# Optimization experiments

Measured on AMD Instinct MI355X. Metric: run time of the kernel, lower is better.

## Reference

```python
import math
import jax, jax.numpy as jnp
import numpy as np

ALPHA, BETA, GAMMA = 1.9, 3.8, 15.2
HEIGHT, WIDTH, SKIP = 32, 32, 1
NUM_HEADS, DIM = 12, 768
HEAD_DIM = DIM // NUM_HEADS


def _piecewise_index_np(rp, alpha, beta, gamma):
    # Eq. (18): identity inside |rp|<=alpha, logarithmic bucketing outside, clipped at beta.
    rp = rp.astype(np.float64)
    rp_abs = np.abs(rp)
    inside = np.round(rp)
    log_part = alpha + np.log(np.maximum(rp_abs, 1e-9) / alpha) / math.log(gamma / alpha) * (beta - alpha)
    outside = np.sign(rp) * np.minimum(np.round(log_part), beta)
    return np.where(rp_abs <= alpha, inside, outside).astype(np.int64)


def _bucket_ids_cross(height, width, skip, alpha, beta, gamma, axis):
    # axis=0 -> CROSS_ROWS, axis=1 -> CROSS_COLS
    rows = np.arange(height)[:, None].repeat(width, 1)
    cols = np.arange(width)[None, :].repeat(height, 0)
    pos = np.stack([rows, cols], 2).reshape(-1, 2)  # [L, 2]
    diff = pos[:, None, axis] - pos[None, :, axis]  # [L, L]
    beta_int = int(beta)
    ids = _piecewise_index_np(diff, alpha, beta, gamma) + beta_int  # in [0, 2*beta_int]
    num_buckets = 2 * beta_int + 1
    L = height * width
    if skip > 0:
        extra = num_buckets
        new_ids = np.full((skip + L, skip + L), extra, dtype=np.int64)
        new_ids[skip:, skip:] = ids
        ids = new_ids
        num_buckets += 1
    return ids.astype(np.int32), num_buckets


def setup_inputs() -> dict:
    key = jax.random.key(0)
    ks = jax.random.split(key, 8)
    N = SKIP + HEIGHT * WIDTH  # 1025
    B = 8
    br, nb = _bucket_ids_cross(HEIGHT, WIDTH, SKIP, ALPHA, BETA, GAMMA, axis=0)
    bc, _ = _bucket_ids_cross(HEIGHT, WIDTH, SKIP, ALPHA, BETA, GAMMA, axis=1)
    w = 0.02
    return {
        "x": jax.random.normal(ks[0], (B, N, DIM), jnp.float32),
        "qkv_w": jax.random.normal(ks[1], (3 * DIM, DIM), jnp.float32) * w,
        "qkv_b": jnp.zeros((3 * DIM,), jnp.float32),
        "proj_w": jax.random.normal(ks[2], (DIM, DIM), jnp.float32) * w,
        "proj_b": jnp.zeros((DIM,), jnp.float32),
        "rpe_rows": jax.random.normal(ks[3], (NUM_HEADS, nb, HEAD_DIM), jnp.float32) * w,
        "rpe_cols": jax.random.normal(ks[4], (NUM_HEADS, nb, HEAD_DIM), jnp.float32) * w,
        "bucket_rows": jnp.asarray(br),
        "bucket_cols": jnp.asarray(bc),
    }


def reference(x, qkv_w, qkv_b, proj_w, proj_b, rpe_rows, rpe_cols, bucket_rows, bucket_cols):
    B, N, C = x.shape
    h = rpe_rows.shape[0]
    d = C // h
    scale = d ** -0.5
    qkv = (x @ qkv_w.T + qkv_b).reshape(B, N, 3, h, d).transpose(2, 0, 3, 1, 4)  # [3,B,h,N,d]
    q, k, v = qkv[0] * scale, qkv[1], qkv[2]
    attn = jnp.einsum('bhid,bhjd->bhij', q, k)  # [B,h,N,N]
    # contextual RPE on keys: project q onto per-head bucket tables, gather per (i,j)
    qt_r = jnp.einsum('bhid,hud->bhiu', q, rpe_rows)  # [B,h,N,nb]
    qt_c = jnp.einsum('bhid,hud->bhiu', q, rpe_cols)
    bias = (jnp.take_along_axis(qt_r, bucket_rows[None, None].astype(jnp.int32), axis=3)
            + jnp.take_along_axis(qt_c, bucket_cols[None, None].astype(jnp.int32), axis=3))
    attn = jax.nn.softmax(attn + bias, axis=-1)
    out = jnp.einsum('bhij,bhjd->bhid', attn, v)
    out = out.transpose(0, 2, 1, 3).reshape(B, N, C)
    return out @ proj_w.T + proj_b
```

## Files before the change

kernel.cpp:

```cpp
#include <hip/hip_runtime.h>

typedef unsigned short u16;
typedef unsigned int   u32;
typedef short  s16x8 __attribute__((ext_vector_type(8)));
typedef float  f32x4 __attribute__((ext_vector_type(4)));

#define B_   8
#define N_   1025
#define H_   12
#define D_   64
#define C_   768
#define NB_  8
#define M_   (B_*N_)
#define QKV_ (3*C_)
#define NEGI -30000.0f
#define LOG2E 1.44269504089f
#define SHIFT2 11.5415603271f
#define CS_  1088

__device__ __forceinline__ float bf2f(u16 u) {
    unsigned int i = ((unsigned int)u) << 16;
    float f; __builtin_memcpy(&f, &i, 4); return f;
}
__device__ __forceinline__ u16 f2bf(float f) {
    unsigned int i; __builtin_memcpy(&i, &f, 4);
    i = (i + 0x7FFFu + ((i >> 16) & 1u)) >> 16;
    return (u16)i;
}
__device__ __forceinline__ float exp2fast(float x) {
#if __has_builtin(__builtin_amdgcn_exp2f)
    return __builtin_amdgcn_exp2f(x);
#else
    float r; asm("v_exp_f32 %0, %1" : "=v"(r) : "v"(x)); return r;
#endif
}

__device__ __forceinline__ void gload_lds16(const u16* gptr, u16* lptr) {
    __builtin_amdgcn_global_load_lds(
        (const __attribute__((address_space(1))) void*)gptr,
        (__attribute__((address_space(3))) void*)lptr, 16, 0, 0);
}

__global__ __launch_bounds__(256)
void cvt_f32_bf16(const float* __restrict__ a, u16* __restrict__ oa, long na,
                  const float* __restrict__ b, u16* __restrict__ ob, long nb,
                  const float* __restrict__ c, u16* __restrict__ oc, long nc)
{
    long t = ((long)blockIdx.x * 256 + threadIdx.x) * 8;
    const float* s; u16* d; long off;
    if (t < na)                 { s = a; d = oa; off = t; }
    else if (t < na + nb)       { s = b; d = ob; off = t - na; }
    else if (t < na + nb + nc)  { s = c; d = oc; off = t - na - nb; }
    else return;
    float4 f0 = *reinterpret_cast<const float4*>(s + off);
    float4 f1 = *reinterpret_cast<const float4*>(s + off + 4);
    u16 tmp[8] = { f2bf(f0.x), f2bf(f0.y), f2bf(f0.z), f2bf(f0.w),
                   f2bf(f1.x), f2bf(f1.y), f2bf(f1.z), f2bf(f1.w) };
    *reinterpret_cast<uint4*>(d + off) = *reinterpret_cast<uint4*>(tmp);
}

__global__ void build_cidx(const int* __restrict__ brow, const int* __restrict__ bcol,
                           unsigned char* __restrict__ cidx) {
    long t = (long)blockIdx.x * 256 + threadIdx.x;
    const long total = (long)CS_ * (CS_ / 4);
    if (t >= total) return;
    int i = (int)(t / (CS_ / 4));
    int k = (int)(t % (CS_ / 4));
    u32 w = 0;
    int p0 = k * 4;
    #pragma unroll
    for (int bnb = 0; bnb < 4; ++bnb) {
        int p = p0 + bnb;
        int jt = p >> 6, rem = p & 63;
        int l = rem >> 2, bn = rem & 3;
        int j = jt * 64 + bn * 16 + l;
        u32 c = 63u;
        if (i < N_ && j < N_) {
            u32 br = (u32)(brow[(size_t)i * N_ + j] & 7);
            u32 bc = (u32)(bcol[(size_t)i * N_ + j] & 7);
            c = (br << 3) | bc;
        }
        w |= c << (8 * bnb);
    }
    ((u32*)cidx)[t] = w;
}

template<int OF32>
__global__ __launch_bounds__(256)
void gemm_bt(const u16* __restrict__ Ap, int lda,
             const u16* __restrict__ Btp,
             const float* __restrict__ bias,
             void* __restrict__ Cout, int ldc,
             int M, int Nn, int K, int scale_cols, float scale_val)
{
    __shared__ u16 As[128][32];
    __shared__ u16 Bs[128][32];
    const int tid  = threadIdx.x;
    const int lane = tid & 63;
    const int wave = tid >> 6;
    const int wm = (wave >> 1) * 64;
    const int wn = (wave & 1) * 64;
    const int m0 = blockIdx.y * 128;
    const int n0 = blockIdx.x * 128;

    const int srow = wave * 16 + (lane >> 2);
    const int scol = (lane & 3) * 8;

    f32x4 acc[4][4] = {};

    for (int k0 = 0; k0 < K; k0 += 32) {
        __syncthreads();
        #pragma unroll
        for (int i = 0; i < 2; ++i) {
            int ar = m0 + i * 64 + srow;
            if (ar > M - 1) ar = M - 1;
            gload_lds16(Ap + (size_t)ar * lda + k0 + scol, &As[i * 64 + wave * 16][0]);
            int br = n0 + i * 64 + srow;
            gload_lds16(Btp + (size_t)br * K + k0 + scol,  &Bs[i * 64 + wave * 16][0]);
        }
        __syncthreads();

        s16x8 af[4], bfv[4];
        #pragma unroll
        for (int qq = 0; qq < 4; ++qq) {
            af[qq]  = *reinterpret_cast<const s16x8*>(&As[wm + qq*16 + (lane & 15)][(lane >> 4) * 8]);
            bfv[qq] = *reinterpret_cast<const s16x8*>(&Bs[wn + qq*16 + (lane & 15)][(lane >> 4) * 8]);
        }
        #pragma unroll
        for (int bm = 0; bm < 4; ++bm)
            #pragma unroll
            for (int bn = 0; bn < 4; ++bn)
                acc[bm][bn] = __builtin_amdgcn_mfma_f32_16x16x32_bf16(af[bm], bfv[bn], acc[bm][bn], 0, 0, 0);
    }

    #pragma unroll
    for (int bm = 0; bm < 4; ++bm) {
        #pragma unroll
        for (int bn = 0; bn < 4; ++bn) {
            int col = n0 + wn + bn*16 + (lane & 15);
            float bv = bias[col];
            float sc = (col < scale_cols) ? scale_val : 1.0f;
            #pragma unroll
            for (int r = 0; r < 4; ++r) {
                int row = m0 + wm + bm*16 + (lane >> 4)*4 + r;
                if (row < M) {
                    float v = (acc[bm][bn][r] + bv) * sc;
                    size_t idx = (size_t)row * ldc + col;
                    if (OF32) ((float*)Cout)[idx] = v;
                    else      ((u16*)Cout)[idx]   = f2bf(v);
                }
            }
        }
    }
}

__global__ __launch_bounds__(256)
void flash_kernel(const u16* __restrict__ qkv,
                  const float* __restrict__ rpe_r, const float* __restrict__ rpe_c,
                  const unsigned char* __restrict__ cidx,
                  u16* __restrict__ aout)
{
    __shared__ u16 Ks[64][72];
    __shared__ u16 Vt[64][72];
    __shared__ u16 Ps[4][16][72];
    __shared__ u16 qtComb[64][72];

    const int tid  = threadIdx.x;
    const int lane = tid & 63;
    const int wave = tid >> 6;
    const int q    = lane >> 4;
    const int l    = lane & 15;
    const int bh = blockIdx.y;
    const int b = bh / H_;
    const int h = bh % H_;
    const int i0 = blockIdx.x * 64;

    float* qtrA = (float*)&Ps[0][0][0];
    float* qtcA = qtrA + 64 * 8;

    {
        int row = tid >> 2;
        int u0  = (tid & 3) * 2;
        int ig = i0 + row;
        float qv[64];
        if (ig < N_) {
            const u16* qrow = &qkv[(size_t)(b * N_ + ig) * QKV_ + h * D_];
            #pragma unroll
            for (int e = 0; e < 8; ++e) {
                uint4 t = *reinterpret_cast<const uint4*>(&qrow[e * 8]);
                s16x8 q8 = *reinterpret_cast<s16x8*>(&t);
                #pragma unroll
                for (int j = 0; j < 8; ++j) qv[e*8 + j] = bf2f((u16)q8[j]);
            }
        } else {
            #pragma unroll
            for (int d = 0; d < 64; ++d) qv[d] = 0.f;
        }
        #pragma unroll
        for (int uu = 0; uu < 2; ++uu) {
            int u = u0 + uu;
            const float4* rr4 = (const float4*)&rpe_r[(size_t)(h * NB_ + u) * D_];
            const float4* rc4 = (const float4*)&rpe_c[(size_t)(h * NB_ + u) * D_];
            float sr = 0.f, sc = 0.f;
            #pragma unroll
            for (int e = 0; e < 16; ++e) {
                float4 a = rr4[e], c4 = rc4[e];
                sr += qv[4*e]*a.x + qv[4*e+1]*a.y + qv[4*e+2]*a.z + qv[4*e+3]*a.w;
                sc += qv[4*e]*c4.x + qv[4*e+1]*c4.y + qv[4*e+2]*c4.z + qv[4*e+3]*c4.w;
            }
            qtrA[row*8 + u] = sr;
            qtcA[row*8 + u] = sc;
        }
    }
    __syncthreads();
    {
        int row = tid >> 2;
        int c0  = (tid & 3) * 16;
        u16 tmp[16];
        #pragma unroll
        for (int cc = 0; cc < 16; ++cc) {
            int c = c0 + cc;
            tmp[cc] = f2bf(qtrA[row*8 + (c >> 3)] + qtcA[row*8 + (c & 7)]);
        }
        *reinterpret_cast<uint4*>(&qtComb[row][c0])     = *reinterpret_cast<uint4*>(&tmp[0]);
        *reinterpret_cast<uint4*>(&qtComb[row][c0 + 8]) = *reinterpret_cast<uint4*>(&tmp[8]);
    }

    s16x8 qf[2];
    {
        int iq = i0 + wave * 16 + l;
        #pragma unroll
        for (int ks = 0; ks < 2; ++ks) {
            uint4 v = make_uint4(0u, 0u, 0u, 0u);
            if (iq < N_)
                v = *reinterpret_cast<const uint4*>(
                    &qkv[(size_t)(b * N_ + iq) * QKV_ + h * D_ + ks * 32 + q * 8]);
            qf[ks] = *reinterpret_cast<s16x8*>(&v);
        }
    }

    float l_part[4] = {0.f, 0.f, 0.f, 0.f};
    f32x4 o_acc[4] = {};

    const int srow = tid >> 3;
    const int g8   = tid & 7;
    const int scol = g8 * 8;
    const int rowq  = wave * 16 + q * 4;
    const int rowq4 = q * 4;

    uint4 kpre[2], vpre[2];
    #pragma unroll
    for (int rr = 0; rr < 2; ++rr) {
        int jg = rr * 32 + srow;
        kpre[rr] = make_uint4(0u,0u,0u,0u); vpre[rr] = make_uint4(0u,0u,0u,0u);
        if (jg < N_) {
            size_t base = (size_t)(b * N_ + jg) * QKV_ + h * D_ + scol;
            kpre[rr] = *reinterpret_cast<const uint4*>(&qkv[base + C_]);
            vpre[rr] = *reinterpret_cast<const uint4*>(&qkv[base + 2 * C_]);
        }
    }

#define SMAX_BN(bn, MASKED_)                                                  \
    {                                                                         \
        const int jbw = (((bn) << 1) | (l >> 3)) ^ q;                         \
        const int sw = (jbw << 3) | (l & 7);                                  \
        _Pragma("unroll")                                                     \
        for (int r = 0; r < 4; ++r) {                                         \
            int c = (cpk[r] >> ((bn) * 8)) & 63;                              \
            float biasv = bf2f(qtComb[rowq + r][c]);                          \
            float lg = s[bn][r] + biasv;                                      \
            if (MASKED_) { if ((j0 + (bn) * 16 + l) >= N_) lg = NEGI; }       \
            float p = exp2fast(lg);                                           \
            l_part[r] += p;                                                   \
            Ps[wave][rowq4 + r][sw] = f2bf(p);                                \
        }                                                                     \
    }

#define PVHALF(ks)                                                            \
    {                                                                         \
        const int qi = (l >> 2) & 3;                                          \
        s16x8 pf = *reinterpret_cast<const s16x8*>(                           \
            &Ps[wave][l][((((ks) << 2) | q) ^ qi) << 3]);                     \
        _Pragma("unroll")                                                     \
        for (int bn = 0; bn < 4; ++bn) {                                      \
            int gd = ((bn << 1) | (l >> 3)) & 7;                              \
            int jb = (((ks) << 2) | q) ^ gd;                                  \
            s16x8 vf = *reinterpret_cast<const s16x8*>(&Vt[bn * 16 + l][jb << 3]); \
            o_acc[bn] = __builtin_amdgcn_mfma_f32_16x16x32_bf16(pf, vf, o_acc[bn], 0, 0, 0); \
        }                                                                     \
    }

    const int nJT = (N_ + 63) / 64;
    for (int jt = 0; jt < nJT; ++jt) {
        const int j0 = jt * 64;

        u32 cpk[4];
        #pragma unroll
        for (int r = 0; r < 4; ++r) {
            int ig = i0 + wave * 16 + q * 4 + r;
            cpk[r] = *reinterpret_cast<const u32*>(&cidx[(size_t)ig * CS_ + j0 + 4 * l]);
        }

        __syncthreads();

        #pragma unroll
        for (int rr = 0; rr < 2; ++rr) {
            int row = rr * 32 + srow;
            *reinterpret_cast<uint4*>(&Ks[row][scol]) = kpre[rr];
            s16x8 v8 = *reinterpret_cast<s16x8*>(&vpre[rr]);
            int base = (((row >> 3) ^ g8) << 3) | (row & 7);
            #pragma unroll
            for (int e = 0; e < 8; ++e) Vt[scol + e][base] = (u16)v8[e];
        }
        #pragma unroll
        for (int rr = 0; rr < 2; ++rr) {
            int jg = (jt + 1) * 64 + rr * 32 + srow;
            kpre[rr] = make_uint4(0u,0u,0u,0u); vpre[rr] = make_uint4(0u,0u,0u,0u);
            if (jg < N_) {
                size_t base = (size_t)(b * N_ + jg) * QKV_ + h * D_ + scol;
                kpre[rr] = *reinterpret_cast<const uint4*>(&qkv[base + C_]);
                vpre[rr] = *reinterpret_cast<const uint4*>(&qkv[base + 2 * C_]);
            }
        }
        __syncthreads();

        f32x4 s[4];
        #pragma unroll
        for (int bn = 0; bn < 4; ++bn)
            s[bn] = (f32x4){-SHIFT2, -SHIFT2, -SHIFT2, -SHIFT2};
        #pragma unroll
        for (int bn = 0; bn < 4; ++bn) {
            #pragma unroll
            for (int ks = 0; ks < 2; ++ks) {
                s16x8 kf = *reinterpret_cast<const s16x8*>(&Ks[bn * 16 + l][ks * 32 + q * 8]);
                s[bn] = __builtin_amdgcn_mfma_f32_16x16x32_bf16(qf[ks], kf, s[bn], 0, 0, 0);
            }
        }

        if (jt < nJT - 1) {
            SMAX_BN(0, 0) SMAX_BN(1, 0)
            PVHALF(0)
            SMAX_BN(2, 0) SMAX_BN(3, 0)
            PVHALF(1)
        } else {
            SMAX_BN(0, 1) SMAX_BN(1, 1)
            PVHALF(0)
            SMAX_BN(2, 1) SMAX_BN(3, 1)
            PVHALF(1)
        }
    }

    #pragma unroll
    for (int r = 0; r < 4; ++r) {
        #pragma unroll
        for (int s2 = 1; s2 < 16; s2 <<= 1)
            l_part[r] += __shfl_xor(l_part[r], s2, 64);
    }
    #pragma unroll
    for (int bn = 0; bn < 4; ++bn) {
        #pragma unroll
        for (int r = 0; r < 4; ++r) {
            int ig = i0 + wave * 16 + q * 4 + r;
            if (ig < N_) {
                float lsum = l_part[r];
                float invl = (lsum > 0.f) ? (1.0f / lsum) : 0.f;
                aout[(size_t)(b * N_ + ig) * C_ + h * D_ + bn * 16 + l] = f2bf(o_acc[bn][r] * invl);
            }
        }
    }
#undef SMAX_BN
#undef PVHALF
}

extern "C" void kernel_launch(void* const* d_in, const int* in_sizes, int n_in,
                              void* d_out, int out_size, void* d_ws, size_t ws_size,
                              hipStream_t stream)
{
    const float* x      = (const float*)d_in[0];
    const float* qkv_w  = (const float*)d_in[1];
    const float* qkv_b  = (const float*)d_in[2];
    const float* proj_w = (const float*)d_in[3];
    const float* proj_b = (const float*)d_in[4];
    const float* rpe_r  = (const float*)d_in[5];
    const float* rpe_c  = (const float*)d_in[6];
    const int*   brow   = (const int*)d_in[7];
    const int*   bcol   = (const int*)d_in[8];

    char* p = (char*)d_ws;
    u16* qkv  = (u16*)p; p += (size_t)M_ * QKV_ * 2;
    u16* xaout = (u16*)p; p += (size_t)M_ * C_ * 2;
    unsigned char* cidx = (unsigned char*)p; p += (size_t)CS_ * CS_;
    u16* w1bf = (u16*)p; p += (size_t)QKV_ * C_ * 2;
    u16* w2bf = (u16*)p;

    const long nx = (long)M_ * C_;
    const long n1 = (long)QKV_ * C_;
    const long n2 = (long)C_ * C_;

    cvt_f32_bf16<<<(int)((nx + n1 + n2) / 8 / 256), 256, 0, stream>>>(
        x, xaout, nx, qkv_w, w1bf, n1, proj_w, w2bf, n2);

    build_cidx<<<((CS_ * (CS_ / 4)) + 255) / 256, 256, 0, stream>>>(brow, bcol, cidx);

    gemm_bt<0><<<dim3(QKV_ / 128, (M_ + 127) / 128), 256, 0, stream>>>(
        xaout, C_, w1bf, qkv_b, qkv, QKV_, M_, QKV_, C_, C_, 0.125f * LOG2E);

    flash_kernel<<<dim3((N_ + 63) / 64, B_ * H_), 256, 0, stream>>>(
        qkv, rpe_r, rpe_c, cidx, xaout);

    gemm_bt<1><<<dim3(C_ / 128, (M_ + 127) / 128), 256, 0, stream>>>(
        xaout, C_, w2bf, proj_b, d_out, C_, M_, C_, C_, 0, 1.0f);
}
```

Measured before the change: 328.8 us.

## Write V transposed from QKV GEMM and read K/V fragments directly from global

The QKV GEMM epilogue now writes V into a separate transposed, padded [B,H,D,1088] buffer and keeps Q and K in a narrower 1536-wide array. The flash kernel drops its shared-memory K and V staging, the register prefetch and two barriers per tile, and loads MFMA fragments straight from global memory (L2/L1). This is meant to remove the LDS transpose and sync cost. In exchange the GEMM does strided scattered stores for V, a small extra kernel zeroes the padding, and global load latency is no longer hidden by prefetching.

Result: slower. 513.5 us (+56.2%).

```diff
diff --git a/kernel.cpp b/kernel.cpp
--- a/kernel.cpp
+++ b/kernel.cpp
@@ -13,6 +13,8 @@
 #define NB_  8
 #define M_   (B_*N_)
 #define QKV_ (3*C_)
+#define QK2_ 1536
+#define VS2_ 1088
 #define NEGI -30000.0f
 #define LOG2E 1.44269504089f
 #define SHIFT2 11.5415603271f
@@ -57,6 +59,16 @@
     u16 tmp[8] = { f2bf(f0.x), f2bf(f0.y), f2bf(f0.z), f2bf(f0.w),
                    f2bf(f1.x), f2bf(f1.y), f2bf(f1.z), f2bf(f1.w) };
     *reinterpret_cast<uint4*>(d + off) = *reinterpret_cast<uint4*>(tmp);
+}
+
+__global__ __launch_bounds__(256)
+void zero_vpad(u16* __restrict__ vT) {
+    const int pad = VS2_ - N_;
+    int t = blockIdx.x * 256 + threadIdx.x;
+    const int total = B_ * H_ * D_ * pad;
+    if (t >= total) return;
+    int rr = t / pad, pp = t % pad;
+    vT[(size_t)rr * VS2_ + N_ + pp] = 0;
 }
 
 __global__ void build_cidx(const int* __restrict__ brow, const int* __restrict__ bcol,
@@ -85,13 +97,14 @@
     ((u32*)cidx)[t] = w;
 }
 
-template<int OF32>
+template<int OF32, int VT>
 __global__ __launch_bounds__(256)
 void gemm_bt(const u16* __restrict__ Ap, int lda,
              const u16* __restrict__ Btp,
              const float* __restrict__ bias,
              void* __restrict__ Cout, int ldc,
-             int M, int Nn, int K, int scale_cols, float scale_val)
+             int M, int Nn, int K, int scale_cols, float scale_val,
+             u16* __restrict__ vt)
 {
     __shared__ u16 As[128][32];
     __shared__ u16 Bs[128][32];
@@ -145,9 +158,16 @@
                 int row = m0 + wm + bm*16 + (lane >> 4)*4 + r;
                 if (row < M) {
                     float v = (acc[bm][bn][r] + bv) * sc;
-                    size_t idx = (size_t)row * ldc + col;
-                    if (OF32) ((float*)Cout)[idx] = v;
-                    else      ((u16*)Cout)[idx]   = f2bf(v);
+                    if (VT && col >= 2 * C_) {
+                        int b2 = row / N_;
+                        int j2 = row - b2 * N_;
+                        int hd = col - 2 * C_;
+                        vt[((size_t)(b2 * (H_ * D_) + hd)) * VS2_ + j2] = f2bf(v);
+                    } else {
+                        size_t idx = (size_t)row * ldc + col;
+                        if (OF32) ((float*)Cout)[idx] = v;
+                        else      ((u16*)Cout)[idx]   = f2bf(v);
+                    }
                 }
             }
         }
@@ -156,12 +176,11 @@
 
 __global__ __launch_bounds__(256)
 void flash_kernel(const u16* __restrict__ qkv,
+                  const u16* __restrict__ vT,
                   const float* __restrict__ rpe_r, const float* __restrict__ rpe_c,
                   const unsigned char* __restrict__ cidx,
                   u16* __restrict__ aout)
 {
-    __shared__ u16 Ks[64][72];
-    __shared__ u16 Vt[64][72];
     __shared__ u16 Ps[4][16][72];
     __shared__ u16 qtComb[64][72];
 
@@ -182,20 +201,8 @@
         int row = tid >> 2;
         int u0  = (tid & 3) * 2;
         int ig = i0 + row;
-        float qv[64];
-        if (ig < N_) {
-            const u16* qrow = &qkv[(size_t)(b * N_ + ig) * QKV_ + h * D_];
-            #pragma unroll
-            for (int e = 0; e < 8; ++e) {
-                uint4 t = *reinterpret_cast<const uint4*>(&qrow[e * 8]);
-                s16x8 q8 = *reinterpret_cast<s16x8*>(&t);
-                #pragma unroll
-                for (int j = 0; j < 8; ++j) qv[e*8 + j] = bf2f((u16)q8[j]);
-            }
-        } else {
-            #pragma unroll
-            for (int d = 0; d < 64; ++d) qv[d] = 0.f;
-        }
+        bool valid = ig < N_;
+        const u16* qrow = &qkv[(size_t)(b * N_ + (valid ? ig : 0)) * QK2_ + h * D_];
         #pragma unroll
         for (int uu = 0; uu < 2; ++uu) {
             int u = u0 + uu;
@@ -203,13 +210,22 @@
             const float4* rc4 = (const float4*)&rpe_c[(size_t)(h * NB_ + u) * D_];
             float sr = 0.f, sc = 0.f;
             #pragma unroll
-            for (int e = 0; e < 16; ++e) {
-                float4 a = rr4[e], c4 = rc4[e];
-                sr += qv[4*e]*a.x + qv[4*e+1]*a.y + qv[4*e+2]*a.z + qv[4*e+3]*a.w;
-                sc += qv[4*e]*c4.x + qv[4*e+1]*c4.y + qv[4*e+2]*c4.z + qv[4*e+3]*c4.w;
+            for (int e2 = 0; e2 < 8; ++e2) {
+                uint4 t = *reinterpret_cast<const uint4*>(&qrow[e2 * 8]);
+                s16x8 q8 = *reinterpret_cast<s16x8*>(&t);
+                float4 a0 = rr4[2*e2], a1 = rr4[2*e2+1];
+                float4 c0 = rc4[2*e2], c1 = rc4[2*e2+1];
+                float f0 = bf2f((u16)q8[0]), f1 = bf2f((u16)q8[1]);
+                float f2 = bf2f((u16)q8[2]), f3 = bf2f((u16)q8[3]);
+                float f4 = bf2f((u16)q8[4]), f5 = bf2f((u16)q8[5]);
+                float f6 = bf2f((u16)q8[6]), f7 = bf2f((u16)q8[7]);
+                sr += f0*a0.x + f1*a0.y + f2*a0.z + f3*a0.w
+                    + f4*a1.x + f5*a1.y + f6*a1.z + f7*a1.w;
+                sc += f0*c0.x + f1*c0.y + f2*c0.z + f3*c0.w
+                    + f4*c1.x + f5*c1.y + f6*c1.z + f7*c1.w;
             }
-            qtrA[row*8 + u] = sr;
-            qtcA[row*8 + u] = sc;
+            qtrA[row*8 + u] = valid ? sr : 0.f;
+            qtcA[row*8 + u] = valid ? sc : 0.f;
         }
     }
     __syncthreads();
@@ -234,31 +250,20 @@
             uint4 v = make_uint4(0u, 0u, 0u, 0u);
             if (iq < N_)
                 v = *reinterpret_cast<const uint4*>(
-                    &qkv[(size_t)(b * N_ + iq) * QKV_ + h * D_ + ks * 32 + q * 8]);
+                    &qkv[(size_t)(b * N_ + iq) * QK2_ + h * D_ + ks * 32 + q * 8]);
             qf[ks] = *reinterpret_cast<s16x8*>(&v);
         }
     }
+    __syncthreads();
 
     float l_part[4] = {0.f, 0.f, 0.f, 0.f};
     f32x4 o_acc[4] = {};
 
-    const int srow = tid >> 3;
-    const int g8   = tid & 7;
-    const int scol = g8 * 8;
     const int rowq  = wave * 16 + q * 4;
     const int rowq4 = q * 4;
 
-    uint4 kpre[2], vpre[2];
-    #pragma unroll
-    for (int rr = 0; rr < 2; ++rr) {
-        int jg = rr * 32 + srow;
-        kpre[rr] = make_uint4(0u,0u,0u,0u); vpre[rr] = make_uint4(0u,0u,0u,0u);
-        if (jg < N_) {
-            size_t base = (size_t)(b * N_ + jg) * QKV_ + h * D_ + scol;
-            kpre[rr] = *reinterpret_cast<const uint4*>(&qkv[base + C_]);
-            vpre[rr] = *reinterpret_cast<const uint4*>(&qkv[base + 2 * C_]);
-        }
-    }
+    const u16* kb = qkv + (size_t)b * N_ * QK2_ + C_ + h * D_ + q * 8;
+    const u16* vb = vT + ((size_t)(b * H_ + h) * D_) * VS2_ + q * 8;
 
 #define SMAX_BN(bn, MASKED_)                                                  \
     {                                                                         \
@@ -283,9 +288,8 @@
             &Ps[wave][l][((((ks) << 2) | q) ^ qi) << 3]);                     \
         _Pragma("unroll")                                                     \
         for (int bn = 0; bn < 4; ++bn) {                                      \
-            int gd = ((bn << 1) | (l >> 3)) & 7;                              \
-            int jb = (((ks) << 2) | q) ^ gd;                                  \
-            s16x8 vf = *reinterpret_cast<const s16x8*>(&Vt[bn * 16 + l][jb << 3]); \
+            s16x8 vf = *reinterpret_cast<const s16x8*>(                       \
+                vb + (size_t)(bn * 16 + l) * VS2_ + j0 + (ks) * 32);          \
             o_acc[bn] = __builtin_amdgcn_mfma_f32_16x16x32_bf16(pf, vf, o_acc[bn], 0, 0, 0); \
         }                                                                     \
     }
@@ -301,38 +305,18 @@
             cpk[r] = *reinterpret_cast<const u32*>(&cidx[(size_t)ig * CS_ + j0 + 4 * l]);
         }
 
-        __syncthreads();
-
-        #pragma unroll
-        for (int rr = 0; rr < 2; ++rr) {
-            int row = rr * 32 + srow;
-            *reinterpret_cast<uint4*>(&Ks[row][scol]) = kpre[rr];
-            s16x8 v8 = *reinterpret_cast<s16x8*>(&vpre[rr]);
-            int base = (((row >> 3) ^ g8) << 3) | (row & 7);
-            #pragma unroll
-            for (int e = 0; e < 8; ++e) Vt[scol + e][base] = (u16)v8[e];
-        }
-        #pragma unroll
-        for (int rr = 0; rr < 2; ++rr) {
-            int jg = (jt + 1) * 64 + rr * 32 + srow;
-            kpre[rr] = make_uint4(0u,0u,0u,0u); vpre[rr] = make_uint4(0u,0u,0u,0u);
-            if (jg < N_) {
-                size_t base = (size_t)(b * N_ + jg) * QKV_ + h * D_ + scol;
-                kpre[rr] = *reinterpret_cast<const uint4*>(&qkv[base + C_]);
-                vpre[rr] = *reinterpret_cast<const uint4*>(&qkv[base + 2 * C_]);
-            }
-        }
-        __syncthreads();
-
         f32x4 s[4];
         #pragma unroll
         for (int bn = 0; bn < 4; ++bn)
             s[bn] = (f32x4){-SHIFT2, -SHIFT2, -SHIFT2, -SHIFT2};
         #pragma unroll
         for (int bn = 0; bn < 4; ++bn) {
+            int jc = j0 + bn * 16 + l;
+            if (jc >= N_) jc = N_ - 1;
+            const u16* kr = kb + (size_t)jc * QK2_;
             #pragma unroll
             for (int ks = 0; ks < 2; ++ks) {
-                s16x8 kf = *reinterpret_cast<const s16x8*>(&Ks[bn * 16 + l][ks * 32 + q * 8]);
+                s16x8 kf = *reinterpret_cast<const s16x8*>(kr + ks * 32);
                 s[bn] = __builtin_amdgcn_mfma_f32_16x16x32_bf16(qf[ks], kf, s[bn], 0, 0, 0);
             }
         }
@@ -387,8 +371,9 @@
     const int*   bcol   = (const int*)d_in[8];
 
     char* p = (char*)d_ws;
-    u16* qkv  = (u16*)p; p += (size_t)M_ * QKV_ * 2;
+    u16* qkv2  = (u16*)p; p += (size_t)M_ * QK2_ * 2;
     u16* xaout = (u16*)p; p += (size_t)M_ * C_ * 2;
+    u16* vT    = (u16*)p; p += (size_t)B_ * H_ * D_ * VS2_ * 2;
     unsigned char* cidx = (unsigned char*)p; p += (size_t)CS_ * CS_;
     u16* w1bf = (u16*)p; p += (size_t)QKV_ * C_ * 2;
     u16* w2bf = (u16*)p;
@@ -400,14 +385,15 @@
     cvt_f32_bf16<<<(int)((nx + n1 + n2) / 8 / 256), 256, 0, stream>>>(
         x, xaout, nx, qkv_w, w1bf, n1, proj_w, w2bf, n2);
 
+    zero_vpad<<<(B_ * H_ * D_ * (VS2_ - N_) + 255) / 256, 256, 0, stream>>>(vT);
     build_cidx<<<((CS_ * (CS_ / 4)) + 255) / 256, 256, 0, stream>>>(brow, bcol, cidx);
 
-    gemm_bt<0><<<dim3(QKV_ / 128, (M_ + 127) / 128), 256, 0, stream>>>(
-        xaout, C_, w1bf, qkv_b, qkv, QKV_, M_, QKV_, C_, C_, 0.125f * LOG2E);
+    gemm_bt<0,1><<<dim3(QKV_ / 128, (M_ + 127) / 128), 256, 0, stream>>>(
+        xaout, C_, w1bf, qkv_b, qkv2, QK2_, M_, QKV_, C_, C_, 0.125f * LOG2E, vT);
 
     flash_kernel<<<dim3((N_ + 63) / 64, B_ * H_), 256, 0, stream>>>(
-        qkv, rpe_r, rpe_c, cidx, xaout);
-
-    gemm_bt<1><<<dim3(C_ / 128, (M_ + 127) / 128), 256, 0, stream>>>(
-        xaout, C_, w2bf, proj_b, d_out, C_, M_, C_, C_, 0, 1.0f);
-}
+        qkv2, vT, rpe_r, rpe_c, cidx, xaout);
+
+    gemm_bt<1,0><<<dim3(C_ / 128, (M_ + 127) / 128), 256, 0, stream>>>(
+        xaout, C_, w2bf, proj_b, d_out, C_, M_, C_, C_, 0, 1.0f, nullptr);
+}
```

## Double flash attention query tile to 128 rows with 512-thread blocks

Applied to the files above, without the earlier changes.

The flash kernel now processes 128 query rows per block with 8 waves, so each K/V tile staged in shared memory is reused by twice as many query rows and each thread loads one K/V row instead of two. The RPE projection prologue streams q in chunks rather than holding a 64-float register array, which lowers register pressure for the new launch bound of 512 threads with 4 blocks per unit. The cidx row index is clamped to stay in bounds for the larger tile. In exchange the grid has half as many blocks (9 per batch-head) with more padded rows in the last tile, and shared memory per block grows.

After: 316.0 us. 3.9% less time.

```diff
diff --git a/kernel.cpp b/kernel.cpp
--- a/kernel.cpp
+++ b/kernel.cpp
@@ -154,7 +154,7 @@
     }
 }
 
-__global__ __launch_bounds__(256)
+__global__ __launch_bounds__(512, 4)
 void flash_kernel(const u16* __restrict__ qkv,
                   const float* __restrict__ rpe_r, const float* __restrict__ rpe_c,
                   const unsigned char* __restrict__ cidx,
@@ -162,8 +162,8 @@
 {
     __shared__ u16 Ks[64][72];
     __shared__ u16 Vt[64][72];
-    __shared__ u16 Ps[4][16][72];
-    __shared__ u16 qtComb[64][72];
+    __shared__ u16 Ps[8][16][72];
+    __shared__ u16 qtComb[128][72];
 
     const int tid  = threadIdx.x;
     const int lane = tid & 63;
@@ -173,29 +173,17 @@
     const int bh = blockIdx.y;
     const int b = bh / H_;
     const int h = bh % H_;
-    const int i0 = blockIdx.x * 64;
+    const int i0 = blockIdx.x * 128;
 
     float* qtrA = (float*)&Ps[0][0][0];
-    float* qtcA = qtrA + 64 * 8;
+    float* qtcA = qtrA + 128 * 8;
 
     {
         int row = tid >> 2;
         int u0  = (tid & 3) * 2;
         int ig = i0 + row;
-        float qv[64];
-        if (ig < N_) {
-            const u16* qrow = &qkv[(size_t)(b * N_ + ig) * QKV_ + h * D_];
-            #pragma unroll
-            for (int e = 0; e < 8; ++e) {
-                uint4 t = *reinterpret_cast<const uint4*>(&qrow[e * 8]);
-                s16x8 q8 = *reinterpret_cast<s16x8*>(&t);
-                #pragma unroll
-                for (int j = 0; j < 8; ++j) qv[e*8 + j] = bf2f((u16)q8[j]);
-            }
-        } else {
-            #pragma unroll
-            for (int d = 0; d < 64; ++d) qv[d] = 0.f;
-        }
+        bool valid = ig < N_;
+        const u16* qrow = &qkv[(size_t)(b * N_ + (valid ? ig : 0)) * QKV_ + h * D_];
         #pragma unroll
         for (int uu = 0; uu < 2; ++uu) {
             int u = u0 + uu;
@@ -203,13 +191,22 @@
             const float4* rc4 = (const float4*)&rpe_c[(size_t)(h * NB_ + u) * D_];
             float sr = 0.f, sc = 0.f;
             #pragma unroll
-            for (int e = 0; e < 16; ++e) {
-                float4 a = rr4[e], c4 = rc4[e];
-                sr += qv[4*e]*a.x + qv[4*e+1]*a.y + qv[4*e+2]*a.z + qv[4*e+3]*a.w;
-                sc += qv[4*e]*c4.x + qv[4*e+1]*c4.y + qv[4*e+2]*c4.z + qv[4*e+3]*c4.w;
+            for (int e2 = 0; e2 < 8; ++e2) {
+                uint4 t = *reinterpret_cast<const uint4*>(&qrow[e2 * 8]);
+                s16x8 q8 = *reinterpret_cast<s16x8*>(&t);
+                float4 a0 = rr4[2*e2], a1 = rr4[2*e2+1];
+                float4 c0 = rc4[2*e2], c1 = rc4[2*e2+1];
+                float f0 = bf2f((u16)q8[0]), f1 = bf2f((u16)q8[1]);
+                float f2 = bf2f((u16)q8[2]), f3 = bf2f((u16)q8[3]);
+                float f4 = bf2f((u16)q8[4]), f5 = bf2f((u16)q8[5]);
+                float f6 = bf2f((u16)q8[6]), f7 = bf2f((u16)q8[7]);
+                sr += f0*a0.x + f1*a0.y + f2*a0.z + f3*a0.w
+                    + f4*a1.x + f5*a1.y + f6*a1.z + f7*a1.w;
+                sc += f0*c0.x + f1*c0.y + f2*c0.z + f3*c0.w
+                    + f4*c1.x + f5*c1.y + f6*c1.z + f7*c1.w;
             }
-            qtrA[row*8 + u] = sr;
-            qtcA[row*8 + u] = sc;
+            qtrA[row*8 + u] = valid ? sr : 0.f;
+            qtcA[row*8 + u] = valid ? sc : 0.f;
         }
     }
     __syncthreads();
@@ -248,15 +245,14 @@
     const int rowq  = wave * 16 + q * 4;
     const int rowq4 = q * 4;
 
-    uint4 kpre[2], vpre[2];
-    #pragma unroll
-    for (int rr = 0; rr < 2; ++rr) {
-        int jg = rr * 32 + srow;
-        kpre[rr] = make_uint4(0u,0u,0u,0u); vpre[rr] = make_uint4(0u,0u,0u,0u);
+    uint4 kpre, vpre;
+    {
+        int jg = srow;
+        kpre = make_uint4(0u,0u,0u,0u); vpre = make_uint4(0u,0u,0u,0u);
         if (jg < N_) {
             size_t base = (size_t)(b * N_ + jg) * QKV_ + h * D_ + scol;
-            kpre[rr] = *reinterpret_cast<const uint4*>(&qkv[base + C_]);
-            vpre[rr] = *reinterpret_cast<const uint4*>(&qkv[base + 2 * C_]);
+            kpre = *reinterpret_cast<const uint4*>(&qkv[base + C_]);
+            vpre = *reinterpret_cast<const uint4*>(&qkv[base + 2 * C_]);
         }
     }
 
@@ -298,28 +294,26 @@
         #pragma unroll
         for (int r = 0; r < 4; ++r) {
             int ig = i0 + wave * 16 + q * 4 + r;
+            if (ig > CS_ - 1) ig = CS_ - 1;
             cpk[r] = *reinterpret_cast<const u32*>(&cidx[(size_t)ig * CS_ + j0 + 4 * l]);
         }
 
         __syncthreads();
 
-        #pragma unroll
-        for (int rr = 0; rr < 2; ++rr) {
-            int row = rr * 32 + srow;
-            *reinterpret_cast<uint4*>(&Ks[row][scol]) = kpre[rr];
-            s16x8 v8 = *reinterpret_cast<s16x8*>(&vpre[rr]);
-            int base = (((row >> 3) ^ g8) << 3) | (row & 7);
+        {
+            *reinterpret_cast<uint4*>(&Ks[srow][scol]) = kpre;
+            s16x8 v8 = *reinterpret_cast<s16x8*>(&vpre);
+            int base = (((srow >> 3) ^ g8) << 3) | (srow & 7);
             #pragma unroll
             for (int e = 0; e < 8; ++e) Vt[scol + e][base] = (u16)v8[e];
         }
-        #pragma unroll
-        for (int rr = 0; rr < 2; ++rr) {
-            int jg = (jt + 1) * 64 + rr * 32 + srow;
-            kpre[rr] = make_uint4(0u,0u,0u,0u); vpre[rr] = make_uint4(0u,0u,0u,0u);
+        {
+            int jg = (jt + 1) * 64 + srow;
+            kpre = make_uint4(0u,0u,0u,0u); vpre = make_uint4(0u,0u,0u,0u);
             if (jg < N_) {
                 size_t base = (size_t)(b * N_ + jg) * QKV_ + h * D_ + scol;
-                kpre[rr] = *reinterpret_cast<const uint4*>(&qkv[base + C_]);
-                vpre[rr] = *reinterpret_cast<const uint4*>(&qkv[base + 2 * C_]);
+                kpre = *reinterpret_cast<const uint4*>(&qkv[base + C_]);
+                vpre = *reinterpret_cast<const uint4*>(&qkv[base + 2 * C_]);
             }
         }
         __syncthreads();
@@ -405,7 +399,7 @@
     gemm_bt<0><<<dim3(QKV_ / 128, (M_ + 127) / 128), 256, 0, stream>>>(
         xaout, C_, w1bf, qkv_b, qkv, QKV_, M_, QKV_, C_, C_, 0.125f * LOG2E);
 
-    flash_kernel<<<dim3((N_ + 63) / 64, B_ * H_), 256, 0, stream>>>(
+    flash_kernel<<<dim3((N_ + 127) / 128, B_ * H_), 512, 0, stream>>>(
         qkv, rpe_r, rpe_c, cidx, xaout);
 
     gemm_bt<1><<<dim3(C_ / 128, (M_ + 127) / 128), 256, 0, stream>>>(
```
